# Performance work log

Hardware: AMD Instinct MI355X
Metric: run time of the kernel (lower is better)

## Reference

```python
import jax, jax.numpy as jnp
import numpy as np

N, D, DPE, H = 4096, 256, 16, 8
HD = D // H
SCALE = HD ** -0.5


def setup_inputs() -> dict:
    key = jax.random.key(0)
    ks = jax.random.split(key, 10)
    s = lambda fan_in: 1.0 / np.sqrt(fan_in)
    return {
        "x": jax.random.normal(ks[0], (N, D), jnp.float32),
        "pe": jax.random.normal(ks[1], (N, DPE), jnp.float32),
        "Wqkv": jax.random.uniform(ks[2], (D, 3 * D), jnp.float32, -s(D), s(D)),
        "bqkv": jax.random.uniform(ks[3], (3 * D,), jnp.float32, -s(D), s(D)),
        "Wpe": jax.random.uniform(ks[4], (DPE, H), jnp.float32, -s(DPE), s(DPE)),
        "bpe": jax.random.uniform(ks[5], (H,), jnp.float32, -s(DPE), s(DPE)),
        "Wout": jax.random.uniform(ks[6], (D, D), jnp.float32, -s(D), s(D)),
        "bout": jax.random.uniform(ks[7], (D,), jnp.float32, -s(D), s(D)),
    }


def reference(x, pe, Wqkv, bqkv, Wpe, bpe, Wout, bout):
    # qkv: [N, 3, H, HD] -> q,k,v each [H, N, HD]
    qkv = (x @ Wqkv + bqkv).reshape(N, 3, H, HD).transpose(1, 2, 0, 3)
    q, k, v = qkv[0], qkv[1], qkv[2]
    # attention scores [H, N, N]
    attn = jnp.einsum("hnd,hmd->hnm", q, k) * SCALE
    # pairwise PE-difference bias: bias[h,i,j] = pe_proj[i,h] - pe_proj[j,h]
    pe_proj = pe @ Wpe + bpe  # [N, H]
    pe_bias = (pe_proj[:, None, :] - pe_proj[None, :, :]).transpose(2, 0, 1)
    attn = jax.nn.softmax(attn + pe_bias, axis=-1)
    # dropout disabled (eval mode, p=0)
    out = jnp.einsum("hnm,hmd->nhd", attn, v).reshape(N, D)
    return out @ Wout + bout
```

## Files before the change

### kernel.cpp

```cpp
#include <hip/hip_runtime.h>
#include <math.h>

#define NN 4096
#define HH 8
constexpr float SCALE = 0.17677669529663687f;
constexpr float LOG2E = 1.4426950408889634f;
constexpr float SC2   = SCALE * LOG2E;

typedef __bf16 bf16;
typedef __bf16 bf16x8 __attribute__((ext_vector_type(8)));
typedef __bf16 bf16x4 __attribute__((ext_vector_type(4)));
typedef __bf16 bf16x2 __attribute__((ext_vector_type(2)));
typedef float  f32x4  __attribute__((ext_vector_type(4)));
typedef unsigned u32;
typedef unsigned u32x4 __attribute__((ext_vector_type(4)));

#define MFMA(a, b, c) __builtin_amdgcn_mfma_f32_16x16x32_bf16((a), (b), (c), 0, 0, 0)

__device__ __forceinline__ u32 pkbf(float lo, float hi) {
    bf16x2 t;
    t[0] = (bf16)lo;
    t[1] = (bf16)hi;
    return __builtin_bit_cast(u32, t);
}

template <int K, int N, bool SCALEQ>
__device__ __forceinline__ void wcast_body(const float* __restrict__ W,
                                           bf16* __restrict__ WhT,
                                           bf16* __restrict__ WlT,
                                           int n0, int k0, int t,
                                           float (*tile)[65]) {
#pragma unroll
    for (int p = 0; p < 16; ++p) {
        const int r = p * 4 + (t >> 6);
        const int c = t & 63;
        tile[r][c] = W[(size_t)(k0 + r) * N + n0 + c];
    }
    __syncthreads();
    const int nr = t >> 2, kc0 = (t & 3) * 16;
    const float sc = (SCALEQ && (n0 + nr) < 256) ? SC2 : 1.0f;
    bf16x8 h[2], l[2];
#pragma unroll
    for (int g = 0; g < 2; ++g)
#pragma unroll
        for (int j = 0; j < 8; ++j) {
            const float v = tile[kc0 + g * 8 + j][nr] * sc;
            const bf16 hh = (bf16)v;
            h[g][j] = hh;
            l[g][j] = (bf16)(v - (float)hh);
        }
    const size_t ob = (size_t)(n0 + nr) * K + k0 + kc0;
    *(bf16x8*)&WhT[ob] = h[0];
    *(bf16x8*)&WhT[ob + 8] = h[1];
    *(bf16x8*)&WlT[ob] = l[0];
    *(bf16x8*)&WlT[ob + 8] = l[1];
}

__global__ __launch_bounds__(256, 2) void gemmqkv_kernel(
    const float* __restrict__ A, const float* __restrict__ Wqkv,
    const float* __restrict__ bqkv,
    const float* __restrict__ pe, const float* __restrict__ Wpe,
    const float* __restrict__ bpe, const float* __restrict__ Wout,
    bf16* __restrict__ Qb, bf16* __restrict__ Kf, bf16* __restrict__ Vf,
    bf16* __restrict__ WouthT, bf16* __restrict__ WoutlT) {
    const int t = threadIdx.x, wave = t >> 6, lane = t & 63;
    const int quad = lane >> 4, i16 = lane & 15;
    const int mb = blockIdx.x, ct = blockIdx.y;

    __shared__ __align__(16) bf16 Bs[32 * 512];
    __shared__ __align__(16) bf16 Ctl[128 * 36];
    __shared__ float eps[128];

    if (ct == 24) {
        if (mb < 16)
            wcast_body<256, 256, false>(Wout, WouthT, WoutlT,
                                        (mb % 4) * 64, (mb / 4) * 64, t,
                                        (float(*)[65]) & Bs[0]);
        return;
    }

    const int m0 = mb * 128 + wave * 32;
    const int n0 = ct * 32;

    {
        const int i16l = lane & 15, ql = lane >> 4;
        const float sc = (ct < 8) ? SC2 : 1.0f;
#pragma unroll
        for (int cc = wave; cc < 16; cc += 4) {
            const int nsi = cc >> 3, kc = cc & 7;
            const int n = n0 + nsi * 16 + i16l;
            const int kk = kc * 32 + ql * 8;
            bf16x8 h, l;
#pragma unroll
            for (int j = 0; j < 8; ++j) {
                const float v = Wqkv[(size_t)(kk + j) * 768 + n] * sc;
                const bf16 hh = (bf16)v;
                h[j] = hh;
                l[j] = (bf16)(v - (float)hh);
            }
            *(bf16x8*)&Bs[cc * 512 + lane * 8] = h;
            *(bf16x8*)&Bs[(cc + 16) * 512 + lane * 8] = l;
        }
    }
    if (ct >= 16 && t < 128) {
        const int h = ct - 16, n = mb * 128 + t;
        float acc = bpe[h];
#pragma unroll
        for (int k = 0; k < 16; ++k) acc += pe[n * 16 + k] * Wpe[k * 8 + h];
        eps[t] = __builtin_amdgcn_exp2f(-acc * LOG2E - 8.0f);
    }

    bf16x8 ah[2][8], al[2][8];
#pragma unroll
    for (int ms = 0; ms < 2; ++ms) {
        const int row = m0 + ms * 16 + i16;
#pragma unroll
        for (int kc = 0; kc < 8; ++kc) {
            const size_t ab = (size_t)row * 256 + kc * 32 + quad * 8;
            const f32x4 u0 = *(const f32x4*)&A[ab];
            const f32x4 u1 = *(const f32x4*)&A[ab + 4];
#pragma unroll
            for (int e = 0; e < 4; ++e) {
                const bf16 h0 = (bf16)u0[e], h1 = (bf16)u1[e];
                ah[ms][kc][e] = h0;
                ah[ms][kc][e + 4] = h1;
                al[ms][kc][e] = (bf16)(u0[e] - (float)h0);
                al[ms][kc][e + 4] = (bf16)(u1[e] - (float)h1);
            }
        }
    }
    __syncthreads();

    f32x4 acc[2][2];
#pragma unroll
    for (int nsi = 0; nsi < 2; ++nsi) {
        acc[nsi][0] = f32x4{0.f, 0.f, 0.f, 0.f};
        acc[nsi][1] = f32x4{0.f, 0.f, 0.f, 0.f};
#pragma unroll
        for (int kc = 0; kc < 8; ++kc) {
            const bf16x8 bh = *(const bf16x8*)&Bs[(nsi * 8 + kc) * 512 + lane * 8];
            const bf16x8 bl = *(const bf16x8*)&Bs[((2 + nsi) * 8 + kc) * 512 + lane * 8];
            acc[nsi][0] = MFMA(ah[0][kc], bh, acc[nsi][0]);
            acc[nsi][0] = MFMA(ah[0][kc], bl, acc[nsi][0]);
            acc[nsi][0] = MFMA(al[0][kc], bh, acc[nsi][0]);
            acc[nsi][1] = MFMA(ah[1][kc], bh, acc[nsi][1]);
            acc[nsi][1] = MFMA(ah[1][kc], bl, acc[nsi][1]);
            acc[nsi][1] = MFMA(al[1][kc], bh, acc[nsi][1]);
        }
    }

    if (ct < 8) {
#pragma unroll
        for (int nsi = 0; nsi < 2; ++nsi) {
            const int n = n0 + nsi * 16 + i16;
            const float b = bqkv[n] * SC2;
#pragma unroll
            for (int ms = 0; ms < 2; ++ms)
#pragma unroll
                for (int r = 0; r < 4; ++r)
                    Qb[(size_t)(m0 + ms * 16 + quad * 4 + r) * 256 + n] =
                        (bf16)(acc[nsi][ms][r] + b);
        }
        return;
    }

#pragma unroll
    for (int nsi = 0; nsi < 2; ++nsi) {
        const int n = n0 + nsi * 16 + i16;
        const float b = bqkv[n];
#pragma unroll
        for (int ms = 0; ms < 2; ++ms)
#pragma unroll
            for (int r = 0; r < 4; ++r)
                Ctl[(wave * 32 + ms * 16 + quad * 4 + r) * 36 + nsi * 16 + i16] =
                    (bf16)(acc[nsi][ms][r] + b);
    }
    __syncthreads();

    if (ct < 16) {
        const int h = ct - 8;
#pragma unroll
        for (int c = wave; c < 8; c += 4) {
            const int half = c >> 2, s = c & 3;
            bf16x8 o;
#pragma unroll
            for (int j = 0; j < 8; ++j)
                o[j] = Ctl[(half * 64 + s * 16 + i16) * 36 + quad * 8 + j];
            *(bf16x8*)&Kf[((size_t)(h * 64 + mb * 2 + half) * 4 + s) * 512 + lane * 8] = o;
        }
    } else {
        const int h = ct - 16;
#pragma unroll
        for (int c = wave; c < 12; c += 4) {
            const int half = c / 6, ch = c % 6;
            const int dt = ch >> 1, kc = ch & 1;
            const int dimp = dt * 16 + i16;
            bf16x8 o;
#pragma unroll
            for (int j = 0; j < 8; ++j) {
                const int key = half * 64 + kc * 32 + quad * 8 + j;
                float v;
                if (dimp < 32)       v = (float)Ctl[key * 36 + dimp] * eps[key];
                else if (dimp == 32) v = eps[key];
                else                 v = 0.f;
                o[j] = (bf16)v;
            }
            *(bf16x8*)&Vf[((size_t)(h * 64 + mb * 2 + half) * 6 + ch) * 512 + lane * 8] = o;
        }
    }
}

template <int NOUT, int NTILE, typename OT>
__global__ __launch_bounds__(256, 2) void gemm3s_kernel(const bf16* __restrict__ Ah,
                                                        const bf16* __restrict__ Al,
                                                        const bf16* __restrict__ BhT,
                                                        const bf16* __restrict__ BlT,
                                                        const float* __restrict__ bias,
                                                        OT* __restrict__ C) {
    constexpr int NS = NTILE / 16;
    const int t = threadIdx.x, wave = t >> 6, lane = t & 63;
    const int quad = lane >> 4, i16 = lane & 15;
    const int m0 = blockIdx.x * 128 + wave * 32;
    const int n0 = blockIdx.y * NTILE;

    __shared__ __align__(16) bf16 Bs[NTILE * 512];

    {
        const int l = t & 63, i16l = l & 15, ql = l >> 4;
#pragma unroll
        for (int c = t >> 6; c < NS * 16; c += 4) {
            const bool lo = c >= NS * 8;
            const int cc = lo ? c - NS * 8 : c;
            const int nsi = cc >> 3, kc = cc & 7;
            const bf16* src = (lo ? BlT : BhT) +
                (size_t)(n0 + nsi * 16 + i16l) * 256 + kc * 32 + ql * 8;
            *(uint4*)&Bs[c * 512 + l * 8] = *(const uint4*)src;
        }
    }

    bf16x8 ah[2][8], al[2][8];
#pragma unroll
    for (int ms = 0; ms < 2; ++ms) {
        const size_t abase = (size_t)(m0 + ms * 16 + i16) * 256 + quad * 8;
#pragma unroll
        for (int kc = 0; kc < 8; ++kc) {
            ah[ms][kc] = *(const bf16x8*)&Ah[abase + kc * 32];
            al[ms][kc] = *(const bf16x8*)&Al[abase + kc * 32];
        }
    }
    __syncthreads();

#pragma unroll
    for (int nsi = 0; nsi < NS; ++nsi) {
        f32x4 acc[2];
        acc[0] = f32x4{0.f, 0.f, 0.f, 0.f};
        acc[1] = f32x4{0.f, 0.f, 0.f, 0.f};
#pragma unroll
        for (int kc = 0; kc < 8; ++kc) {
            const bf16x8 bh = *(const bf16x8*)&Bs[(nsi * 8 + kc) * 512 + lane * 8];
            const bf16x8 bl = *(const bf16x8*)&Bs[((NS + nsi) * 8 + kc) * 512 + lane * 8];
            acc[0] = MFMA(ah[0][kc], bh, acc[0]);
            acc[0] = MFMA(ah[0][kc], bl, acc[0]);
            acc[0] = MFMA(al[0][kc], bh, acc[0]);
            acc[1] = MFMA(ah[1][kc], bh, acc[1]);
            acc[1] = MFMA(ah[1][kc], bl, acc[1]);
            acc[1] = MFMA(al[1][kc], bh, acc[1]);
        }
        const int n = n0 + nsi * 16 + i16;
        const float b = bias[n];
#pragma unroll
        for (int ms = 0; ms < 2; ++ms)
#pragma unroll
            for (int r = 0; r < 4; ++r)
                C[(size_t)(m0 + ms * 16 + quad * 4 + r) * NOUT + n] = (OT)(acc[ms][r] + b);
    }
}

__global__ __launch_bounds__(512, 4) void attn_kernel(const bf16* __restrict__ Qb,
                                                      const bf16* __restrict__ Kf,
                                                      const bf16* __restrict__ Vf,
                                                      bf16* __restrict__ aoh,
                                                      bf16* __restrict__ aol) {
    const int t = threadIdx.x, w = t >> 6, lane = t & 63;
    const int quad = lane >> 4, i16 = lane & 15;
    const int qb = blockIdx.y, h = blockIdx.x;

    __shared__ __align__(16) float M[8][2112];

    const int q0 = qb * 64;
    bf16x8 qf[4];
#pragma unroll
    for (int qs = 0; qs < 4; ++qs)
        qf[qs] = *(const bf16x8*)&Qb[(size_t)(q0 + qs * 16 + i16) * 256 + h * 32 + quad * 8];

    f32x4 o[3][4];
#pragma unroll
    for (int dt = 0; dt < 3; ++dt)
#pragma unroll
        for (int qs = 0; qs < 4; ++qs) o[dt][qs] = f32x4{0.f, 0.f, 0.f, 0.f};

    const bf16* kb = Kf + (size_t)(h * 64) * 2048 + lane * 8;
    const bf16* vb = Vf + (size_t)(h * 64) * 3072 + lane * 8;

    const int kt0 = w * 8;
    for (int it = 0; it < 8; ++it) {
        const int kt = kt0 + it;
        bf16x8 kcur[4];
#pragma unroll
        for (int s = 0; s < 4; ++s)
            kcur[s] = *(const bf16x8*)&kb[((size_t)kt * 4 + s) * 512];

        const f32x4 z = {0.f, 0.f, 0.f, 0.f};
        u32x4 P[4][2];
#pragma unroll
        for (int qh = 0; qh < 2; ++qh) {
            f32x4 sf[2][4];
#pragma unroll
            for (int ks = 0; ks < 4; ++ks) {
                sf[0][ks] = MFMA(kcur[ks], qf[qh * 2 + 0], z);
                sf[1][ks] = MFMA(kcur[ks], qf[qh * 2 + 1], z);
            }
#pragma unroll
            for (int qi = 0; qi < 2; ++qi) {
                const int qs = qh * 2 + qi;
#pragma unroll
                for (int h2 = 0; h2 < 2; ++h2) {
                    const f32x4 s0 = sf[qi][2 * h2 + 0];
                    const f32x4 s1 = sf[qi][2 * h2 + 1];
                    u32 a = pkbf(__builtin_amdgcn_exp2f(s0[0]),
                                 __builtin_amdgcn_exp2f(s0[1]));
                    u32 b = pkbf(__builtin_amdgcn_exp2f(s0[2]),
                                 __builtin_amdgcn_exp2f(s0[3]));
                    u32 c = pkbf(__builtin_amdgcn_exp2f(s1[0]),
                                 __builtin_amdgcn_exp2f(s1[1]));
                    u32 d = pkbf(__builtin_amdgcn_exp2f(s1[2]),
                                 __builtin_amdgcn_exp2f(s1[3]));
                    asm("v_permlane32_swap_b32 %0, %1" : "+v"(a), "+v"(c));
                    asm("v_permlane16_swap_b32 %0, %1" : "+v"(a), "+v"(c));
                    asm("v_permlane32_swap_b32 %0, %1" : "+v"(b), "+v"(d));
                    asm("v_permlane16_swap_b32 %0, %1" : "+v"(b), "+v"(d));
                    P[qs][h2] = u32x4{a, b, c, d};
                }
            }
        }

        bf16x8 vv[6];
#pragma unroll
        for (int c = 0; c < 6; ++c)
            vv[c] = *(const bf16x8*)&vb[((size_t)kt * 6 + c) * 512];

#pragma unroll
        for (int qs = 0; qs < 4; ++qs) {
            const bf16x8 pb0 = __builtin_bit_cast(bf16x8, P[qs][0]);
            const bf16x8 pb1 = __builtin_bit_cast(bf16x8, P[qs][1]);
#pragma unroll
            for (int dt = 0; dt < 3; ++dt) {
                o[dt][qs] = MFMA(vv[dt * 2 + 0], pb0, o[dt][qs]);
                o[dt][qs] = MFMA(vv[dt * 2 + 1], pb1, o[dt][qs]);
            }
        }
    }

    {
        float* myo = &M[w][0];
#pragma unroll
        for (int qs = 0; qs < 4; ++qs) {
            *(f32x4*)&myo[(qs * 64 + lane) * 8 + 0] = o[0][qs];
            *(f32x4*)&myo[(qs * 64 + lane) * 8 + 4] = o[1][qs];
        }
        if (quad == 0) {
#pragma unroll
            for (int qs = 0; qs < 4; ++qs)
                myo[2048 + qs * 16 + i16] = o[2][qs][0];
        }
    }
    __syncthreads();
    if (w < 4) {
        f32x4 a0 = {0.f, 0.f, 0.f, 0.f}, a1 = {0.f, 0.f, 0.f, 0.f};
        float lsum = 0.f;
#pragma unroll
        for (int ww = 0; ww < 8; ++ww) {
            const float* p = &M[ww][0];
            a0 += *(const f32x4*)&p[(w * 64 + lane) * 8 + 0];
            a1 += *(const f32x4*)&p[(w * 64 + lane) * 8 + 4];
            if (lane < 16) lsum += p[2048 + w * 16 + lane];
        }
        const float linv = 1.0f / __shfl(lsum, i16, 64);
        const int row = q0 + w * 16 + i16;
#pragma unroll
        for (int dt = 0; dt < 2; ++dt) {
            const f32x4 src = dt ? a1 : a0;
            bf16x4 hi, lo;
#pragma unroll
            for (int r = 0; r < 4; ++r) {
                const float v = src[r] * linv;
                hi[r] = (bf16)v;
                lo[r] = (bf16)(v - (float)hi[r]);
            }
            const size_t ob = (size_t)row * 256 + h * 32 + dt * 16 + quad * 4;
            *(bf16x4*)&aoh[ob] = hi;
            *(bf16x4*)&aol[ob] = lo;
        }
    }
}

extern "C" void kernel_launch(void* const* d_in, const int* in_sizes, int n_in,
                              void* d_out, int out_size, void* d_ws, size_t ws_size,
                              hipStream_t stream) {
    const float* x    = (const float*)d_in[0];
    const float* pe   = (const float*)d_in[1];
    const float* Wqkv = (const float*)d_in[2];
    const float* bqkv = (const float*)d_in[3];
    const float* Wpe  = (const float*)d_in[4];
    const float* bpe  = (const float*)d_in[5];
    const float* Wout = (const float*)d_in[6];
    const float* bout = (const float*)d_in[7];
    float* out = (float*)d_out;

    char* ws = (char*)d_ws;
    bf16*  WouthT  = (bf16*)(ws + 786432);
    bf16*  WoutlT  = (bf16*)(ws + 917504);
    bf16*  Qb      = (bf16*)(ws + 1048576);
    bf16*  Kf      = (bf16*)(ws + 3145728);
    bf16*  Vf      = (bf16*)(ws + 5242880);
    bf16*  aoh     = (bf16*)(ws + 8388608);
    bf16*  aol     = (bf16*)(ws + 10485760);

    gemmqkv_kernel<<<dim3(32, 25), 256, 0, stream>>>(x, Wqkv, bqkv,
                                                     pe, Wpe, bpe, Wout,
                                                     Qb, Kf, Vf, WouthT, WoutlT);
    attn_kernel<<<dim3(HH, NN / 64), 512, 0, stream>>>(Qb, Kf, Vf, aoh, aol);
    gemm3s_kernel<256, 16, float><<<dim3(32, 16), 256, 0, stream>>>(aoh, aol, WouthT, WoutlT, bout, out);
}
```

Before: 124.2 us.

## Reuse split-bf16 activation tiles across Q, K, V panels per block

Each QKV GEMM block now computes all three projections (Q, K, V) for one head instead of one panel. The block converts its 128-row activation tile to hi/lo bf16 once rather than three times, and double-buffers weight panel staging in shared memory so the next panel loads while the current one is computed. The grid shrinks from 800 to 256 blocks, and the Wout cast work is folded into the g==7 blocks. This trades fewer redundant activation reads and conversions for less parallelism, longer serial blocks, more shared memory per block (which could lower occupancy), and extra barriers.

```diff
diff --git a/kernel.cpp b/kernel.cpp
--- a/kernel.cpp
+++ b/kernel.cpp
@@ -65,26 +65,18 @@
     bf16* __restrict__ WouthT, bf16* __restrict__ WoutlT) {
     const int t = threadIdx.x, wave = t >> 6, lane = t & 63;
     const int quad = lane >> 4, i16 = lane & 15;
-    const int mb = blockIdx.x, ct = blockIdx.y;
-
-    __shared__ __align__(16) bf16 Bs[32 * 512];
+    const int mb = blockIdx.x, g = blockIdx.y;
+
+    __shared__ __align__(16) bf16 Bs[2][32 * 512];
     __shared__ __align__(16) bf16 Ctl[128 * 36];
     __shared__ float eps[128];
 
-    if (ct == 24) {
-        if (mb < 16)
-            wcast_body<256, 256, false>(Wout, WouthT, WoutlT,
-                                        (mb % 4) * 64, (mb / 4) * 64, t,
-                                        (float(*)[65]) & Bs[0]);
-        return;
-    }
-
     const int m0 = mb * 128 + wave * 32;
-    const int n0 = ct * 32;
-
-    {
+
+    auto stage_panel = [&](bf16* bs, int ct) {
         const int i16l = lane & 15, ql = lane >> 4;
         const float sc = (ct < 8) ? SC2 : 1.0f;
+        const int n0 = ct * 32;
 #pragma unroll
         for (int cc = wave; cc < 16; cc += 4) {
             const int nsi = cc >> 3, kc = cc & 7;
@@ -98,17 +90,10 @@
                 h[j] = hh;
                 l[j] = (bf16)(v - (float)hh);
             }
-            *(bf16x8*)&Bs[cc * 512 + lane * 8] = h;
-            *(bf16x8*)&Bs[(cc + 16) * 512 + lane * 8] = l;
-        }
-    }
-    if (ct >= 16 && t < 128) {
-        const int h = ct - 16, n = mb * 128 + t;
-        float acc = bpe[h];
-#pragma unroll
-        for (int k = 0; k < 16; ++k) acc += pe[n * 16 + k] * Wpe[k * 8 + h];
-        eps[t] = __builtin_amdgcn_exp2f(-acc * LOG2E - 8.0f);
-    }
+            *(bf16x8*)&bs[cc * 512 + lane * 8] = h;
+            *(bf16x8*)&bs[(cc + 16) * 512 + lane * 8] = l;
+        }
+    };
 
     bf16x8 ah[2][8], al[2][8];
 #pragma unroll
@@ -129,27 +114,41 @@
             }
         }
     }
-    __syncthreads();
-
-    f32x4 acc[2][2];
-#pragma unroll
-    for (int nsi = 0; nsi < 2; ++nsi) {
-        acc[nsi][0] = f32x4{0.f, 0.f, 0.f, 0.f};
-        acc[nsi][1] = f32x4{0.f, 0.f, 0.f, 0.f};
-#pragma unroll
-        for (int kc = 0; kc < 8; ++kc) {
-            const bf16x8 bh = *(const bf16x8*)&Bs[(nsi * 8 + kc) * 512 + lane * 8];
-            const bf16x8 bl = *(const bf16x8*)&Bs[((2 + nsi) * 8 + kc) * 512 + lane * 8];
-            acc[nsi][0] = MFMA(ah[0][kc], bh, acc[nsi][0]);
-            acc[nsi][0] = MFMA(ah[0][kc], bl, acc[nsi][0]);
-            acc[nsi][0] = MFMA(al[0][kc], bh, acc[nsi][0]);
-            acc[nsi][1] = MFMA(ah[1][kc], bh, acc[nsi][1]);
-            acc[nsi][1] = MFMA(ah[1][kc], bl, acc[nsi][1]);
-            acc[nsi][1] = MFMA(al[1][kc], bh, acc[nsi][1]);
-        }
-    }
-
-    if (ct < 8) {
+
+    auto run_tile = [&](const bf16* bs, f32x4 (&acc)[2][2]) {
+#pragma unroll
+        for (int nsi = 0; nsi < 2; ++nsi) {
+            acc[nsi][0] = f32x4{0.f, 0.f, 0.f, 0.f};
+            acc[nsi][1] = f32x4{0.f, 0.f, 0.f, 0.f};
+#pragma unroll
+            for (int kc = 0; kc < 8; ++kc) {
+                const bf16x8 bh = *(const bf16x8*)&bs[(nsi * 8 + kc) * 512 + lane * 8];
+                const bf16x8 bl = *(const bf16x8*)&bs[((2 + nsi) * 8 + kc) * 512 + lane * 8];
+                acc[nsi][0] = MFMA(ah[0][kc], bh, acc[nsi][0]);
+                acc[nsi][0] = MFMA(ah[0][kc], bl, acc[nsi][0]);
+                acc[nsi][0] = MFMA(al[0][kc], bh, acc[nsi][0]);
+                acc[nsi][1] = MFMA(ah[1][kc], bh, acc[nsi][1]);
+                acc[nsi][1] = MFMA(ah[1][kc], bl, acc[nsi][1]);
+                acc[nsi][1] = MFMA(al[1][kc], bh, acc[nsi][1]);
+            }
+        }
+    };
+
+    stage_panel(Bs[0], g);
+    if (t < 128) {
+        const int n = mb * 128 + t;
+        float acc = bpe[g];
+#pragma unroll
+        for (int k = 0; k < 16; ++k) acc += pe[n * 16 + k] * Wpe[k * 8 + g];
+        eps[t] = __builtin_amdgcn_exp2f(-acc * LOG2E - 8.0f);
+    }
+    __syncthreads();
+
+    stage_panel(Bs[1], 8 + g);
+    {
+        f32x4 acc[2][2];
+        run_tile(Bs[0], acc);
+        const int n0 = g * 32;
 #pragma unroll
         for (int nsi = 0; nsi < 2; ++nsi) {
             const int n = n0 + nsi * 16 + i16;
@@ -161,24 +160,26 @@
                     Qb[(size_t)(m0 + ms * 16 + quad * 4 + r) * 256 + n] =
                         (bf16)(acc[nsi][ms][r] + b);
         }
-        return;
-    }
-
-#pragma unroll
-    for (int nsi = 0; nsi < 2; ++nsi) {
-        const int n = n0 + nsi * 16 + i16;
-        const float b = bqkv[n];
-#pragma unroll
-        for (int ms = 0; ms < 2; ++ms)
-#pragma unroll
-            for (int r = 0; r < 4; ++r)
-                Ctl[(wave * 32 + ms * 16 + quad * 4 + r) * 36 + nsi * 16 + i16] =
-                    (bf16)(acc[nsi][ms][r] + b);
-    }
-    __syncthreads();
-
-    if (ct < 16) {
-        const int h = ct - 8;
+    }
+    __syncthreads();
+
+    stage_panel(Bs[0], 16 + g);
+    {
+        f32x4 acc[2][2];
+        run_tile(Bs[1], acc);
+        const int n0 = (8 + g) * 32;
+#pragma unroll
+        for (int nsi = 0; nsi < 2; ++nsi) {
+            const int n = n0 + nsi * 16 + i16;
+            const float b = bqkv[n];
+#pragma unroll
+            for (int ms = 0; ms < 2; ++ms)
+#pragma unroll
+                for (int r = 0; r < 4; ++r)
+                    Ctl[(wave * 32 + ms * 16 + quad * 4 + r) * 36 + nsi * 16 + i16] =
+                        (bf16)(acc[nsi][ms][r] + b);
+        }
+        __syncthreads();
 #pragma unroll
         for (int c = wave; c < 8; c += 4) {
             const int half = c >> 2, s = c & 3;
@@ -186,10 +187,27 @@
 #pragma unroll
             for (int j = 0; j < 8; ++j)
                 o[j] = Ctl[(half * 64 + s * 16 + i16) * 36 + quad * 8 + j];
-            *(bf16x8*)&Kf[((size_t)(h * 64 + mb * 2 + half) * 4 + s) * 512 + lane * 8] = o;
-        }
-    } else {
-        const int h = ct - 16;
+            *(bf16x8*)&Kf[((size_t)(g * 64 + mb * 2 + half) * 4 + s) * 512 + lane * 8] = o;
+        }
+    }
+    __syncthreads();
+
+    {
+        f32x4 acc[2][2];
+        run_tile(Bs[0], acc);
+        const int n0 = (16 + g) * 32;
+#pragma unroll
+        for (int nsi = 0; nsi < 2; ++nsi) {
+            const int n = n0 + nsi * 16 + i16;
+            const float b = bqkv[n];
+#pragma unroll
+            for (int ms = 0; ms < 2; ++ms)
+#pragma unroll
+                for (int r = 0; r < 4; ++r)
+                    Ctl[(wave * 32 + ms * 16 + quad * 4 + r) * 36 + nsi * 16 + i16] =
+                        (bf16)(acc[nsi][ms][r] + b);
+        }
+        __syncthreads();
 #pragma unroll
         for (int c = wave; c < 12; c += 4) {
             const int half = c / 6, ch = c % 6;
@@ -205,8 +223,15 @@
                 else                 v = 0.f;
                 o[j] = (bf16)v;
             }
-            *(bf16x8*)&Vf[((size_t)(h * 64 + mb * 2 + half) * 6 + ch) * 512 + lane * 8] = o;
-        }
+            *(bf16x8*)&Vf[((size_t)(g * 64 + mb * 2 + half) * 6 + ch) * 512 + lane * 8] = o;
+        }
+    }
+
+    if (g == 7 && mb < 16) {
+        __syncthreads();
+        wcast_body<256, 256, false>(Wout, WouthT, WoutlT,
+                                    (mb % 4) * 64, (mb / 4) * 64, t,
+                                    (float(*)[65]) & Bs[0][0]);
     }
 }
 
@@ -426,9 +451,9 @@
     bf16*  aoh     = (bf16*)(ws + 8388608);
     bf16*  aol     = (bf16*)(ws + 10485760);
 
-    gemmqkv_kernel<<<dim3(32, 25), 256, 0, stream>>>(x, Wqkv, bqkv,
-                                                     pe, Wpe, bpe, Wout,
-                                                     Qb, Kf, Vf, WouthT, WoutlT);
+    gemmqkv_kernel<<<dim3(32, 8), 256, 0, stream>>>(x, Wqkv, bqkv,
+                                                    pe, Wpe, bpe, Wout,
+                                                    Qb, Kf, Vf, WouthT, WoutlT);
     attn_kernel<<<dim3(HH, NN / 64), 512, 0, stream>>>(Qb, Kf, Vf, aoh, aol);
     gemm3s_kernel<256, 16, float><<<dim3(32, 16), 256, 0, stream>>>(aoh, aol, WouthT, WoutlT, bout, out);
 }
```

Result: faster. 121.5 us (-2.2%).
